# Performance work log

Measured on AMD Instinct MI355X. Metric: run time of the kernel, lower is better.

Reference implementation:

```python
import jax, jax.numpy as jnp
import numpy as np

BASE_BITS = 17            # tokens < 2**17; pack n-gram tuple into one int64
NGRAM_SIZES = (2, 3)      # sorted(ngram_to_size.keys())
TABLE_SIZE = 100000       # ngram_to_size[n]
ID_OFFSET = 4             # vocab ids start at 4 in the original
B, S, VOCAB = 256, 16384, 50000


def _encode_windows(x, n):
    """x: [B,S] int tokens -> [B,S] int64, each entry encodes the left-padded
    n-gram window (t[i-n+1],...,t[i]) exactly like the original tuple key."""
    b, s = x.shape
    padded = jnp.pad(x.astype(jnp.int64), ((0, 0), (n - 1, 0)))  # constant 0 pad, as in np.pad
    enc = jnp.zeros((b, s), dtype=jnp.int64)
    for i in range(n):  # tiny fixed loop over window size
        enc = (enc << BASE_BITS) | padded[:, i:i + s]
    return enc


def _lookup(enc, keys, vals):
    """dict.get(tuple(window), 0) as sorted-array hash-probe: searchsorted + verify."""
    flat = enc.reshape(-1)
    idx = jnp.clip(jnp.searchsorted(keys, flat), 0, keys.shape[0] - 1)
    hit = keys[idx] == flat
    return jnp.where(hit, vals[idx], 0).reshape(enc.shape)


def setup_inputs() -> dict:
    rng = np.random.default_rng(0)
    x = rng.integers(0, VOCAB, size=(B, S), dtype=np.int64)
    inp = {"x": jnp.asarray(x)}
    xj = jnp.asarray(x)
    for n in NGRAM_SIZES:
        # Build vocab tables from n-grams actually present so lookups hit,
        # mirroring update_from_batch() having seen similar data.
        enc = np.asarray(_encode_windows(xj, n)).reshape(-1)
        uniq = np.unique(enc)
        take = min(TABLE_SIZE, uniq.size)
        keys = np.sort(rng.choice(uniq, size=take, replace=False)).astype(np.int64)
        vals = (rng.permutation(take) + ID_OFFSET).astype(np.int64)  # ids 4..take+3
        inp[f"keys{n}"] = jnp.asarray(keys)
        inp[f"vals{n}"] = jnp.asarray(vals)
    return inp


def reference(x, keys2, vals2, keys3, vals3):
    tables = {2: (keys2, vals2), 3: (keys3, vals3)}
    # encode_token_ngrams + stack_ngrams -> [len(NGRAM_SIZES), B, S]
    outs = [_lookup(_encode_windows(x, n), *tables[n]) for n in NGRAM_SIZES]
    return jnp.stack(outs, axis=0)
```

## Files before the change

kernel.cpp:

```cpp
#include <hip/hip_runtime.h>

#define BASE_BITS 17
#define BUCKET_LOG 16
#define NBUCKETS (1u << BUCKET_LOG)
#define NSLOTS (NBUCKETS * 4u)
#define SLOT_MASK (NSLOTS - 1u)
#define BUCKET_MASK (NBUCKETS - 1u)
#define EMPTY 0xFFFFFFFFu

typedef int  iv4 __attribute__((ext_vector_type(4)));
typedef unsigned uv4 __attribute__((ext_vector_type(4)));

__device__ __forceinline__ unsigned bucket_of(unsigned k) {
    return (k * 2654435761u) >> (32 - BUCKET_LOG);
}

__device__ __forceinline__ int match4(uv4 q, unsigned e, unsigned b) {
    int slot = -1;
    slot = (q.w == e) ? (int)(b * 4u + 3u) : slot;
    slot = (q.z == e) ? (int)(b * 4u + 2u) : slot;
    slot = (q.y == e) ? (int)(b * 4u + 1u) : slot;
    slot = (q.x == e) ? (int)(b * 4u + 0u) : slot;
    if (slot >= 0) return slot;
    unsigned mx = max(max(q.x, q.y), max(q.z, q.w));
    return (mx == EMPTY) ? -2 : -1;
}

__global__ void detect_dtype_kernel(const unsigned* __restrict__ xw,
                                    int* __restrict__ flags) {
    __shared__ int nz;
    if (threadIdx.x == 0) nz = 0;
    __syncthreads();
    if (xw[2 * threadIdx.x + 1] != 0u) atomicOr(&nz, 1);
    __syncthreads();
    if (threadIdx.x == 0) { flags[0] = nz ? 0 : ~0; flags[1] = 0; }
}

__global__ void build_hash_kernel(const int* __restrict__ keys2,
                                  const int* __restrict__ vals2, int n2,
                                  const int* __restrict__ keys3,
                                  const int* __restrict__ vals3, int n3,
                                  const unsigned* __restrict__ xw,
                                  unsigned* __restrict__ K2, int* __restrict__ V2,
                                  unsigned* __restrict__ K3, int* __restrict__ V3,
                                  int* __restrict__ flags) {
    int i = blockIdx.x * blockDim.x + threadIdx.x;
    if (i < 256 && xw[2 * i + 1] != 0u) atomicAnd(&flags[0], 0);

    const int* keys; const int* vals; unsigned* K; int* V; int idx;
    if (i < n2)           { keys = keys2; vals = vals2; K = K2; V = V2; idx = i; }
    else if (i < n2 + n3) { keys = keys3; vals = vals3; K = K3; V = V3; idx = i - n2; }
    else return;
    unsigned k = (unsigned)keys[idx];
    if (k == EMPTY) { atomicAnd(&flags[1], 0); return; }
    unsigned slot = bucket_of(k) * 4u;
    for (;;) {
        unsigned prev = atomicCAS(&K[slot], EMPTY, k);
        if (prev == EMPTY) { V[slot] = vals[idx]; break; }
        slot = (slot + 1u) & SLOT_MASK;
    }
}

template <typename K>
__device__ __forceinline__ int lower_bound(const K* __restrict__ keys, int n, K key) {
    int lo = 0, hi = n;
    while (lo < hi) {
        int mid = (lo + hi) >> 1;
        if (keys[mid] < key) lo = mid + 1; else hi = mid;
    }
    return lo;
}

template <typename K>
__device__ __forceinline__ K bprobe(const K* __restrict__ keys,
                                    const K* __restrict__ vals, int n, K key) {
    int idx = lower_bound(keys, n, key);
    if (idx >= n) idx = n - 1;
    return (keys[idx] == key) ? vals[idx] : (K)0;
}

__global__ __launch_bounds__(256) void ngram_hash_kernel(
    const void* __restrict__ xv,
    const unsigned* __restrict__ K2, const int* __restrict__ V2,
    const unsigned* __restrict__ K3, const int* __restrict__ V3,
    const void* __restrict__ k2v, const void* __restrict__ v2v,
    const void* __restrict__ k3v, const void* __restrict__ v3v,
    void* __restrict__ outv,
    int n2, int n3, int S, int total, const int* __restrict__ flags)
{
    int gid = blockIdx.x * blockDim.x + threadIdx.x;
    int base = gid * 4;
    if (base >= total) return;
    int f0 = flags[0], f1 = flags[1];

    if (f0 != 0) {
        const long long* x = (const long long*)xv;
        long long* out = (long long*)outv;
        for (int i = 0; i < 4 && base + i < total; ++i) {
            int g = base + i;
            int s = g & (S - 1);
            long long t2 = x[g];
            long long t1 = (s >= 1) ? x[g - 1] : 0ll;
            long long t0 = (s >= 2) ? x[g - 2] : 0ll;
            long long e2 = (t1 << BASE_BITS) | t2;
            long long e3 = (((t0 << BASE_BITS) | t1) << BASE_BITS) | t2;
            out[g]         = bprobe((const long long*)k2v, (const long long*)v2v, n2, e2);
            out[total + g] = bprobe((const long long*)k3v, (const long long*)v3v, n3, e3);
        }
        return;
    }
    if (f1 == 0) {
        const int* x = (const int*)xv;
        int* out = (int*)outv;
        for (int i = 0; i < 4 && base + i < total; ++i) {
            int g = base + i;
            int s = g & (S - 1);
            unsigned t2 = (unsigned)x[g];
            unsigned t1 = (s >= 1) ? (unsigned)x[g - 1] : 0u;
            unsigned t0 = (s >= 2) ? (unsigned)x[g - 2] : 0u;
            int e2 = (int)((t1 << BASE_BITS) | t2);
            int e3 = (int)((((t0 << BASE_BITS) | t1) << BASE_BITS) | t2);
            out[g]         = bprobe((const int*)k2v, (const int*)v2v, n2, e2);
            out[total + g] = bprobe((const int*)k3v, (const int*)v3v, n3, e3);
        }
        return;
    }

    const int* x = (const int*)xv;
    iv4 xq = __builtin_nontemporal_load(&((const iv4*)x)[gid]);
    int sb = base & (S - 1);
    unsigned t[6];
    t[0] = (sb != 0) ? (unsigned)x[base - 2] : 0u;
    t[1] = (sb != 0) ? (unsigned)x[base - 1] : 0u;
    t[2] = (unsigned)xq.x; t[3] = (unsigned)xq.y;
    t[4] = (unsigned)xq.z; t[5] = (unsigned)xq.w;

    unsigned e[8], b[8];
    #pragma unroll
    for (int i = 0; i < 4; ++i) {
        unsigned t0 = t[i], t1 = t[i + 1], t2 = t[i + 2];
        e[i]     = (t1 << BASE_BITS) | t2;
        e[i + 4] = (((t0 << BASE_BITS) | t1) << BASE_BITS) | t2;
    }
    #pragma unroll
    for (int i = 0; i < 8; ++i) b[i] = bucket_of(e[i]);

    const uv4* KB2 = (const uv4*)K2;
    const uv4* KB3 = (const uv4*)K3;

    const uv4* a0 = KB2 + b[0]; const uv4* a1 = KB2 + b[1];
    const uv4* a2 = KB2 + b[2]; const uv4* a3 = KB2 + b[3];
    const uv4* a4 = KB3 + b[4]; const uv4* a5 = KB3 + b[5];
    const uv4* a6 = KB3 + b[6]; const uv4* a7 = KB3 + b[7];
    uv4 q0, q1, q2, q3, q4, q5, q6, q7;
    asm volatile(
        "global_load_dwordx4 %0, %8, off\n\t"
        "global_load_dwordx4 %1, %9, off\n\t"
        "global_load_dwordx4 %2, %10, off\n\t"
        "global_load_dwordx4 %3, %11, off\n\t"
        "global_load_dwordx4 %4, %12, off\n\t"
        "global_load_dwordx4 %5, %13, off\n\t"
        "global_load_dwordx4 %6, %14, off\n\t"
        "global_load_dwordx4 %7, %15, off\n\t"
        "s_waitcnt vmcnt(0)"
        : "=&v"(q0), "=&v"(q1), "=&v"(q2), "=&v"(q3),
          "=&v"(q4), "=&v"(q5), "=&v"(q6), "=&v"(q7)
        : "v"(a0), "v"(a1), "v"(a2), "v"(a3),
          "v"(a4), "v"(a5), "v"(a6), "v"(a7)
        : "memory");

    int st[8];
    st[0] = match4(q0, e[0], b[0]);
    st[1] = match4(q1, e[1], b[1]);
    st[2] = match4(q2, e[2], b[2]);
    st[3] = match4(q3, e[3], b[3]);
    st[4] = match4(q4, e[4], b[4]);
    st[5] = match4(q5, e[5], b[5]);
    st[6] = match4(q6, e[6], b[6]);
    st[7] = match4(q7, e[7], b[7]);

    bool cont = false;
    #pragma unroll
    for (int i = 0; i < 8; ++i) cont |= (st[i] == -1);
    while (__any(cont)) {
        #pragma unroll
        for (int i = 0; i < 8; ++i) {
            if (st[i] == -1) {
                b[i] = (b[i] + 1u) & BUCKET_MASK;
                uv4 nq = (i < 4 ? KB2 : KB3)[b[i]];
                st[i] = match4(nq, e[i], b[i]);
            }
        }
        cont = false;
        #pragma unroll
        for (int i = 0; i < 8; ++i) cont |= (st[i] == -1);
    }

    int r[8];
    #pragma unroll
    for (int i = 0; i < 8; ++i)
        r[i] = (st[i] >= 0) ? (i < 4 ? V2 : V3)[st[i]] : 0;

    iv4 o2 = { r[0], r[1], r[2], r[3] };
    iv4 o3 = { r[4], r[5], r[6], r[7] };
    __builtin_nontemporal_store(o2, &((iv4*)outv)[gid]);
    __builtin_nontemporal_store(o3, &((iv4*)outv)[total / 4 + gid]);
}

extern "C" void kernel_launch(void* const* d_in, const int* in_sizes, int n_in,
                              void* d_out, int out_size, void* d_ws, size_t ws_size,
                              hipStream_t stream) {
    const void* x  = d_in[0];
    const void* k2 = d_in[1];
    const void* v2 = d_in[2];
    const void* k3 = d_in[3];
    const void* v3 = d_in[4];
    int n2 = in_sizes[1];
    int n3 = in_sizes[3];
    int total = in_sizes[0];
    int S = 16384;

    int* flags = (int*)d_ws;
    size_t key_bytes = (size_t)NSLOTS * 4;
    size_t need = 256 + 4 * key_bytes;

    int block = 256;
    int grid = (total / 4 + block - 1) / block;

    if (ws_size >= need) {
        unsigned* K2 = (unsigned*)((char*)d_ws + 256);
        unsigned* K3 = K2 + NSLOTS;
        int* V2 = (int*)(K3 + NSLOTS);
        int* V3 = V2 + NSLOTS;

        (void)hipMemsetAsync(d_ws, 0xFF, 256 + 2 * key_bytes, stream);

        build_hash_kernel<<<(n2 + n3 + 255) / 256, 256, 0, stream>>>(
            (const int*)k2, (const int*)v2, n2,
            (const int*)k3, (const int*)v3, n3,
            (const unsigned*)x, K2, V2, K3, V3, flags);

        ngram_hash_kernel<<<grid, block, 0, stream>>>(
            x, K2, V2, K3, V3, k2, v2, k3, v3, d_out, n2, n3, S, total, flags);
    } else {
        detect_dtype_kernel<<<1, 256, 0, stream>>>((const unsigned*)x, flags);
        ngram_hash_kernel<<<grid, block, 0, stream>>>(
            x, nullptr, nullptr, nullptr, nullptr,
            k2, v2, k3, v3, d_out, n2, n3, S, total, flags);
    }
}
```

Before: 95.09 us.

## Add shared-memory Bloom filter to skip hash probes and use persistent grid

The build kernel now also fills a 2^18-bit Bloom filter per n-gram table. Each block of the lookup kernel copies both filters (64 KB total) into shared memory. Lanes whose key is definitely absent point their hash-bucket load at a fixed dummy address and skip matching and further probing. The lookup kernel switches to a fixed 1024-block grid-stride loop. The change trades fewer scattered bucket reads for a per-block 64 KB filter copy, heavy LDS use that limits occupancy, and an extra LDS lookup per key.

```diff
diff --git a/kernel.cpp b/kernel.cpp
--- a/kernel.cpp
+++ b/kernel.cpp
@@ -8,11 +8,17 @@
 #define BUCKET_MASK (NBUCKETS - 1u)
 #define EMPTY 0xFFFFFFFFu
 
+#define BF_LOG 18
+#define BF_WORDS (1u << (BF_LOG - 5))
+
 typedef int  iv4 __attribute__((ext_vector_type(4)));
 typedef unsigned uv4 __attribute__((ext_vector_type(4)));
 
 __device__ __forceinline__ unsigned bucket_of(unsigned k) {
     return (k * 2654435761u) >> (32 - BUCKET_LOG);
+}
+__device__ __forceinline__ unsigned bloom_of(unsigned k) {
+    return (k * 0x9E3779B1u) >> (32 - BF_LOG);
 }
 
 __device__ __forceinline__ int match4(uv4 q, unsigned e, unsigned b) {
@@ -43,16 +49,20 @@
                                   const unsigned* __restrict__ xw,
                                   unsigned* __restrict__ K2, int* __restrict__ V2,
                                   unsigned* __restrict__ K3, int* __restrict__ V3,
+                                  unsigned* __restrict__ BF2,
+                                  unsigned* __restrict__ BF3,
                                   int* __restrict__ flags) {
     int i = blockIdx.x * blockDim.x + threadIdx.x;
     if (i < 256 && xw[2 * i + 1] != 0u) atomicAnd(&flags[0], 0);
 
-    const int* keys; const int* vals; unsigned* K; int* V; int idx;
-    if (i < n2)           { keys = keys2; vals = vals2; K = K2; V = V2; idx = i; }
-    else if (i < n2 + n3) { keys = keys3; vals = vals3; K = K3; V = V3; idx = i - n2; }
+    const int* keys; const int* vals; unsigned* K; int* V; unsigned* BF; int idx;
+    if (i < n2)           { keys = keys2; vals = vals2; K = K2; V = V2; BF = BF2; idx = i; }
+    else if (i < n2 + n3) { keys = keys3; vals = vals3; K = K3; V = V3; BF = BF3; idx = i - n2; }
     else return;
     unsigned k = (unsigned)keys[idx];
     if (k == EMPTY) { atomicAnd(&flags[1], 0); return; }
+    unsigned h = bloom_of(k);
+    atomicAnd(&BF[h >> 5], ~(1u << (h & 31u)));
     unsigned slot = bucket_of(k) * 4u;
     for (;;) {
         unsigned prev = atomicCAS(&K[slot], EMPTY, k);
@@ -83,128 +93,183 @@
     const void* __restrict__ xv,
     const unsigned* __restrict__ K2, const int* __restrict__ V2,
     const unsigned* __restrict__ K3, const int* __restrict__ V3,
+    const unsigned* __restrict__ gBF2, const unsigned* __restrict__ gBF3,
     const void* __restrict__ k2v, const void* __restrict__ v2v,
     const void* __restrict__ k3v, const void* __restrict__ v3v,
     void* __restrict__ outv,
     int n2, int n3, int S, int total, const int* __restrict__ flags)
 {
-    int gid = blockIdx.x * blockDim.x + threadIdx.x;
-    int base = gid * 4;
-    if (base >= total) return;
+    int tid0 = blockIdx.x * blockDim.x + threadIdx.x;
+    int nthreads = gridDim.x * blockDim.x;
+    int ntask = (total + 3) / 4;
     int f0 = flags[0], f1 = flags[1];
 
     if (f0 != 0) {
         const long long* x = (const long long*)xv;
         long long* out = (long long*)outv;
-        for (int i = 0; i < 4 && base + i < total; ++i) {
-            int g = base + i;
-            int s = g & (S - 1);
-            long long t2 = x[g];
-            long long t1 = (s >= 1) ? x[g - 1] : 0ll;
-            long long t0 = (s >= 2) ? x[g - 2] : 0ll;
-            long long e2 = (t1 << BASE_BITS) | t2;
-            long long e3 = (((t0 << BASE_BITS) | t1) << BASE_BITS) | t2;
-            out[g]         = bprobe((const long long*)k2v, (const long long*)v2v, n2, e2);
-            out[total + g] = bprobe((const long long*)k3v, (const long long*)v3v, n3, e3);
+        for (int task = tid0; task < ntask; task += nthreads) {
+            int base = task * 4;
+            for (int i = 0; i < 4 && base + i < total; ++i) {
+                int g = base + i;
+                int s = g & (S - 1);
+                long long t2 = x[g];
+                long long t1 = (s >= 1) ? x[g - 1] : 0ll;
+                long long t0 = (s >= 2) ? x[g - 2] : 0ll;
+                long long e2 = (t1 << BASE_BITS) | t2;
+                long long e3 = (((t0 << BASE_BITS) | t1) << BASE_BITS) | t2;
+                out[g]         = bprobe((const long long*)k2v, (const long long*)v2v, n2, e2);
+                out[total + g] = bprobe((const long long*)k3v, (const long long*)v3v, n3, e3);
+            }
         }
         return;
     }
     if (f1 == 0) {
         const int* x = (const int*)xv;
         int* out = (int*)outv;
-        for (int i = 0; i < 4 && base + i < total; ++i) {
-            int g = base + i;
-            int s = g & (S - 1);
-            unsigned t2 = (unsigned)x[g];
-            unsigned t1 = (s >= 1) ? (unsigned)x[g - 1] : 0u;
-            unsigned t0 = (s >= 2) ? (unsigned)x[g - 2] : 0u;
-            int e2 = (int)((t1 << BASE_BITS) | t2);
-            int e3 = (int)((((t0 << BASE_BITS) | t1) << BASE_BITS) | t2);
-            out[g]         = bprobe((const int*)k2v, (const int*)v2v, n2, e2);
-            out[total + g] = bprobe((const int*)k3v, (const int*)v3v, n3, e3);
+        for (int task = tid0; task < ntask; task += nthreads) {
+            int base = task * 4;
+            for (int i = 0; i < 4 && base + i < total; ++i) {
+                int g = base + i;
+                int s = g & (S - 1);
+                unsigned t2 = (unsigned)x[g];
+                unsigned t1 = (s >= 1) ? (unsigned)x[g - 1] : 0u;
+                unsigned t0 = (s >= 2) ? (unsigned)x[g - 2] : 0u;
+                int e2 = (int)((t1 << BASE_BITS) | t2);
+                int e3 = (int)((((t0 << BASE_BITS) | t1) << BASE_BITS) | t2);
+                out[g]         = bprobe((const int*)k2v, (const int*)v2v, n2, e2);
+                out[total + g] = bprobe((const int*)k3v, (const int*)v3v, n3, e3);
+            }
         }
         return;
     }
 
+    __shared__ unsigned bf2[BF_WORDS];
+    __shared__ unsigned bf3[BF_WORDS];
+    {
+        const uv4* s2 = (const uv4*)gBF2;
+        const uv4* s3 = (const uv4*)gBF3;
+        uv4* d2 = (uv4*)bf2;
+        uv4* d3 = (uv4*)bf3;
+        for (unsigned w = threadIdx.x; w < BF_WORDS / 4; w += 256) {
+            d2[w] = s2[w];
+            d3[w] = s3[w];
+        }
+    }
+    __syncthreads();
+
     const int* x = (const int*)xv;
-    iv4 xq = __builtin_nontemporal_load(&((const iv4*)x)[gid]);
-    int sb = base & (S - 1);
-    unsigned t[6];
-    t[0] = (sb != 0) ? (unsigned)x[base - 2] : 0u;
-    t[1] = (sb != 0) ? (unsigned)x[base - 1] : 0u;
-    t[2] = (unsigned)xq.x; t[3] = (unsigned)xq.y;
-    t[4] = (unsigned)xq.z; t[5] = (unsigned)xq.w;
-
-    unsigned e[8], b[8];
-    #pragma unroll
-    for (int i = 0; i < 4; ++i) {
-        unsigned t0 = t[i], t1 = t[i + 1], t2 = t[i + 2];
-        e[i]     = (t1 << BASE_BITS) | t2;
-        e[i + 4] = (((t0 << BASE_BITS) | t1) << BASE_BITS) | t2;
-    }
-    #pragma unroll
-    for (int i = 0; i < 8; ++i) b[i] = bucket_of(e[i]);
-
     const uv4* KB2 = (const uv4*)K2;
     const uv4* KB3 = (const uv4*)K3;
 
-    const uv4* a0 = KB2 + b[0]; const uv4* a1 = KB2 + b[1];
-    const uv4* a2 = KB2 + b[2]; const uv4* a3 = KB2 + b[3];
-    const uv4* a4 = KB3 + b[4]; const uv4* a5 = KB3 + b[5];
-    const uv4* a6 = KB3 + b[6]; const uv4* a7 = KB3 + b[7];
-    uv4 q0, q1, q2, q3, q4, q5, q6, q7;
-    asm volatile(
-        "global_load_dwordx4 %0, %8, off\n\t"
-        "global_load_dwordx4 %1, %9, off\n\t"
-        "global_load_dwordx4 %2, %10, off\n\t"
-        "global_load_dwordx4 %3, %11, off\n\t"
-        "global_load_dwordx4 %4, %12, off\n\t"
-        "global_load_dwordx4 %5, %13, off\n\t"
-        "global_load_dwordx4 %6, %14, off\n\t"
-        "global_load_dwordx4 %7, %15, off\n\t"
-        "s_waitcnt vmcnt(0)"
-        : "=&v"(q0), "=&v"(q1), "=&v"(q2), "=&v"(q3),
-          "=&v"(q4), "=&v"(q5), "=&v"(q6), "=&v"(q7)
-        : "v"(a0), "v"(a1), "v"(a2), "v"(a3),
-          "v"(a4), "v"(a5), "v"(a6), "v"(a7)
-        : "memory");
-
-    int st[8];
-    st[0] = match4(q0, e[0], b[0]);
-    st[1] = match4(q1, e[1], b[1]);
-    st[2] = match4(q2, e[2], b[2]);
-    st[3] = match4(q3, e[3], b[3]);
-    st[4] = match4(q4, e[4], b[4]);
-    st[5] = match4(q5, e[5], b[5]);
-    st[6] = match4(q6, e[6], b[6]);
-    st[7] = match4(q7, e[7], b[7]);
-
-    bool cont = false;
-    #pragma unroll
-    for (int i = 0; i < 8; ++i) cont |= (st[i] == -1);
-    while (__any(cont)) {
+    for (int task = tid0; task < ntask; task += nthreads) {
+        int base = task * 4;
+        if (base + 3 >= total) {
+            int* out = (int*)outv;
+            for (int i = 0; i < 4 && base + i < total; ++i) {
+                int g = base + i;
+                int s = g & (S - 1);
+                unsigned t2 = (unsigned)x[g];
+                unsigned t1 = (s >= 1) ? (unsigned)x[g - 1] : 0u;
+                unsigned t0 = (s >= 2) ? (unsigned)x[g - 2] : 0u;
+                unsigned e2 = (t1 << BASE_BITS) | t2;
+                unsigned e3 = (((t0 << BASE_BITS) | t1) << BASE_BITS) | t2;
+                unsigned bb2 = bucket_of(e2), bb3 = bucket_of(e3);
+                int s2v = match4(KB2[bb2], e2, bb2);
+                while (s2v == -1) { bb2 = (bb2 + 1u) & BUCKET_MASK; s2v = match4(KB2[bb2], e2, bb2); }
+                int s3v = match4(KB3[bb3], e3, bb3);
+                while (s3v == -1) { bb3 = (bb3 + 1u) & BUCKET_MASK; s3v = match4(KB3[bb3], e3, bb3); }
+                out[g]         = (s2v >= 0) ? V2[s2v] : 0;
+                out[total + g] = (s3v >= 0) ? V3[s3v] : 0;
+            }
+            continue;
+        }
+
+        iv4 xq = __builtin_nontemporal_load(&((const iv4*)x)[task]);
+        int sb = base & (S - 1);
+        unsigned t[6];
+        t[0] = (sb != 0) ? (unsigned)x[base - 2] : 0u;
+        t[1] = (sb != 0) ? (unsigned)x[base - 1] : 0u;
+        t[2] = (unsigned)xq.x; t[3] = (unsigned)xq.y;
+        t[4] = (unsigned)xq.z; t[5] = (unsigned)xq.w;
+
+        unsigned e[8], b[8];
+        bool maybe[8];
+        #pragma unroll
+        for (int i = 0; i < 4; ++i) {
+            unsigned t0 = t[i], t1 = t[i + 1], t2 = t[i + 2];
+            e[i]     = (t1 << BASE_BITS) | t2;
+            e[i + 4] = (((t0 << BASE_BITS) | t1) << BASE_BITS) | t2;
+        }
         #pragma unroll
         for (int i = 0; i < 8; ++i) {
-            if (st[i] == -1) {
-                b[i] = (b[i] + 1u) & BUCKET_MASK;
-                uv4 nq = (i < 4 ? KB2 : KB3)[b[i]];
-                st[i] = match4(nq, e[i], b[i]);
-            }
-        }
-        cont = false;
+            b[i] = bucket_of(e[i]);
+            unsigned h = bloom_of(e[i]);
+            unsigned w = (i < 4 ? bf2 : bf3)[h >> 5];
+            maybe[i] = ((w >> (h & 31u)) & 1u) == 0u;
+        }
+
+        const uv4* a0 = maybe[0] ? KB2 + b[0] : KB2;
+        const uv4* a1 = maybe[1] ? KB2 + b[1] : KB2;
+        const uv4* a2 = maybe[2] ? KB2 + b[2] : KB2;
+        const uv4* a3 = maybe[3] ? KB2 + b[3] : KB2;
+        const uv4* a4 = maybe[4] ? KB3 + b[4] : KB3;
+        const uv4* a5 = maybe[5] ? KB3 + b[5] : KB3;
+        const uv4* a6 = maybe[6] ? KB3 + b[6] : KB3;
+        const uv4* a7 = maybe[7] ? KB3 + b[7] : KB3;
+        uv4 q0, q1, q2, q3, q4, q5, q6, q7;
+        asm volatile(
+            "global_load_dwordx4 %0, %8, off\n\t"
+            "global_load_dwordx4 %1, %9, off\n\t"
+            "global_load_dwordx4 %2, %10, off\n\t"
+            "global_load_dwordx4 %3, %11, off\n\t"
+            "global_load_dwordx4 %4, %12, off\n\t"
+            "global_load_dwordx4 %5, %13, off\n\t"
+            "global_load_dwordx4 %6, %14, off\n\t"
+            "global_load_dwordx4 %7, %15, off\n\t"
+            "s_waitcnt vmcnt(0)"
+            : "=&v"(q0), "=&v"(q1), "=&v"(q2), "=&v"(q3),
+              "=&v"(q4), "=&v"(q5), "=&v"(q6), "=&v"(q7)
+            : "v"(a0), "v"(a1), "v"(a2), "v"(a3),
+              "v"(a4), "v"(a5), "v"(a6), "v"(a7)
+            : "memory");
+
+        int st[8];
+        st[0] = maybe[0] ? match4(q0, e[0], b[0]) : -2;
+        st[1] = maybe[1] ? match4(q1, e[1], b[1]) : -2;
+        st[2] = maybe[2] ? match4(q2, e[2], b[2]) : -2;
+        st[3] = maybe[3] ? match4(q3, e[3], b[3]) : -2;
+        st[4] = maybe[4] ? match4(q4, e[4], b[4]) : -2;
+        st[5] = maybe[5] ? match4(q5, e[5], b[5]) : -2;
+        st[6] = maybe[6] ? match4(q6, e[6], b[6]) : -2;
+        st[7] = maybe[7] ? match4(q7, e[7], b[7]) : -2;
+
+        bool cont = false;
         #pragma unroll
         for (int i = 0; i < 8; ++i) cont |= (st[i] == -1);
-    }
-
-    int r[8];
-    #pragma unroll
-    for (int i = 0; i < 8; ++i)
-        r[i] = (st[i] >= 0) ? (i < 4 ? V2 : V3)[st[i]] : 0;
-
-    iv4 o2 = { r[0], r[1], r[2], r[3] };
-    iv4 o3 = { r[4], r[5], r[6], r[7] };
-    __builtin_nontemporal_store(o2, &((iv4*)outv)[gid]);
-    __builtin_nontemporal_store(o3, &((iv4*)outv)[total / 4 + gid]);
+        while (__any(cont)) {
+            #pragma unroll
+            for (int i = 0; i < 8; ++i) {
+                if (st[i] == -1) {
+                    b[i] = (b[i] + 1u) & BUCKET_MASK;
+                    uv4 nq = (i < 4 ? KB2 : KB3)[b[i]];
+                    st[i] = match4(nq, e[i], b[i]);
+                }
+            }
+            cont = false;
+            #pragma unroll
+            for (int i = 0; i < 8; ++i) cont |= (st[i] == -1);
+        }
+
+        int r[8];
+        #pragma unroll
+        for (int i = 0; i < 8; ++i)
+            r[i] = (st[i] >= 0) ? (i < 4 ? V2 : V3)[st[i]] : 0;
+
+        iv4 o2 = { r[0], r[1], r[2], r[3] };
+        iv4 o3 = { r[4], r[5], r[6], r[7] };
+        __builtin_nontemporal_store(o2, &((iv4*)outv)[task]);
+        __builtin_nontemporal_store(o3, &((iv4*)outv)[total / 4 + task]);
+    }
 }
 
 extern "C" void kernel_launch(void* const* d_in, const int* in_sizes, int n_in,
@@ -222,30 +287,31 @@
 
     int* flags = (int*)d_ws;
     size_t key_bytes = (size_t)NSLOTS * 4;
-    size_t need = 256 + 4 * key_bytes;
-
-    int block = 256;
-    int grid = (total / 4 + block - 1) / block;
+    size_t bf_bytes  = (size_t)BF_WORDS * 4;
+    size_t need = 256 + 2 * key_bytes + 2 * bf_bytes + 2 * key_bytes;
 
     if (ws_size >= need) {
-        unsigned* K2 = (unsigned*)((char*)d_ws + 256);
-        unsigned* K3 = K2 + NSLOTS;
-        int* V2 = (int*)(K3 + NSLOTS);
+        unsigned* K2  = (unsigned*)((char*)d_ws + 256);
+        unsigned* K3  = K2 + NSLOTS;
+        unsigned* BF2 = K3 + NSLOTS;
+        unsigned* BF3 = BF2 + BF_WORDS;
+        int* V2 = (int*)(BF3 + BF_WORDS);
         int* V3 = V2 + NSLOTS;
 
-        (void)hipMemsetAsync(d_ws, 0xFF, 256 + 2 * key_bytes, stream);
+        (void)hipMemsetAsync(d_ws, 0xFF, 256 + 2 * key_bytes + 2 * bf_bytes, stream);
 
         build_hash_kernel<<<(n2 + n3 + 255) / 256, 256, 0, stream>>>(
             (const int*)k2, (const int*)v2, n2,
             (const int*)k3, (const int*)v3, n3,
-            (const unsigned*)x, K2, V2, K3, V3, flags);
-
-        ngram_hash_kernel<<<grid, block, 0, stream>>>(
-            x, K2, V2, K3, V3, k2, v2, k3, v3, d_out, n2, n3, S, total, flags);
+            (const unsigned*)x, K2, V2, K3, V3, BF2, BF3, flags);
+
+        ngram_hash_kernel<<<1024, 256, 0, stream>>>(
+            x, K2, V2, K3, V3, BF2, BF3, k2, v2, k3, v3,
+            d_out, n2, n3, S, total, flags);
     } else {
         detect_dtype_kernel<<<1, 256, 0, stream>>>((const unsigned*)x, flags);
-        ngram_hash_kernel<<<grid, block, 0, stream>>>(
-            x, nullptr, nullptr, nullptr, nullptr,
+        ngram_hash_kernel<<<1024, 256, 0, stream>>>(
+            x, nullptr, nullptr, nullptr, nullptr, nullptr, nullptr,
             k2, v2, k3, v3, d_out, n2, n3, S, total, flags);
     }
 }
```

After: 109.7 us. +15.3%, slower.
